# Kernel optimization log

Hardware: AMD Instinct MI355X
Metric: run time of the kernel (lower is better)

The kernel has to match this reference:

```python
import jax, jax.numpy as jnp
import numpy as np

T, B, I, H, O = 4096, 256, 2, 32, 1


def setup_inputs() -> dict:
    key = jax.random.key(0)
    ks = jax.random.split(key, 8)
    s = 1.0 / np.sqrt(H)  # torch GRU/Linear init scale
    u = lambda k, shape: jax.random.uniform(k, shape, jnp.float32, -s, s)
    return {
        "x": jax.random.normal(ks[0], (T, B, I), jnp.float32),
        "w_ih": u(ks[1], (3 * H, I)),   # rows ordered [r, z, n] as in torch
        "w_hh": u(ks[2], (3 * H, H)),
        "b_ih": u(ks[3], (3 * H,)),
        "b_hh": u(ks[4], (3 * H,)),
        "w_fc": u(ks[5], (O, H)),
        "b_fc": u(ks[6], (O,)),
    }


def _gru_all_hidden(x, w_ih, w_hh, b_ih, b_hh):
    # Precompute input projections for all steps in one big GEMM: (T,B,3H)
    xg = jnp.einsum('tbi,gi->tbg', x, w_ih) + b_ih

    def step(h, xg_t):
        hg = h @ w_hh.T + b_hh                      # (B,3H)
        xr, xz, xn = jnp.split(xg_t, 3, axis=-1)
        hr, hz, hn = jnp.split(hg, 3, axis=-1)
        r = jax.nn.sigmoid(xr + hr)
        z = jax.nn.sigmoid(xz + hz)
        n = jnp.tanh(xn + r * hn)
        h_new = (1.0 - z) * n + z * h
        return h_new, h_new

    h0 = jnp.zeros((x.shape[1], w_hh.shape[1]), x.dtype)
    _, hs = jax.lax.scan(step, h0, xg)
    return hs                                       # (T,B,H)


def reference(x, w_ih, w_hh, b_ih, b_hh, w_fc, b_fc):
    hs = _gru_all_hidden(x, w_ih, w_hh, b_ih, b_hh)  # (T,B,H)
    # Faithful to the source: output[:, -1, :] with batch_first=False picks
    # the last batch element's hidden state at every timestep -> (T,H)
    out = hs[:, -1, :]
    return out @ w_fc.T + b_fc                       # (T,O)
```

## Files before the change

### kernel.cpp

```cpp
#include <hip/hip_runtime.h>


#define TT 4096

__device__ __forceinline__ float rl(float v, int l) {
    return __int_as_float(__builtin_amdgcn_readlane(__float_as_int(v), l));
}
__device__ __forceinline__ float fexp2(float x) { return __builtin_amdgcn_exp2f(x); }
__device__ __forceinline__ float frcp(float x)  { return __builtin_amdgcn_rcpf(x); }

#define NLOG2E  (-1.44269504088896340736f)
#define TLOG2E  ( 2.88539008177792681472f)

__global__ __launch_bounds__(64, 1)
__attribute__((amdgpu_waves_per_eu(1, 1)))
void gru_seq(const float* __restrict__ x,
             const float* __restrict__ w_ih,
             const float* __restrict__ w_hh,
             const float* __restrict__ b_ih,
             const float* __restrict__ b_hh,
             float* __restrict__ hbuf)
{
    const int lane = threadIdx.x;
    const int low  = lane & 31;
    const bool hi  = lane >= 32;
    const int row0 = lane;
    const int row1 = 64 + low;

    float w0a[32], w1a[32];
#pragma unroll
    for (int j = 0; j < 32; ++j) w0a[j] = w_hh[row0 * 32 + j] * NLOG2E;
#pragma unroll
    for (int j = 0; j < 32; ++j) w1a[j] = w_hh[row1 * 32 + j] * TLOG2E;
#pragma unroll
    for (int j = 0; j < 32; ++j) asm("" : "+v"(w0a[j]));
#pragma unroll
    for (int j = 0; j < 32; ++j) asm("" : "+v"(w1a[j]));

    const float wi00 = w_ih[row0 * 2 + 0] * NLOG2E;
    const float wi01 = w_ih[row0 * 2 + 1] * NLOG2E;
    const float wi10 = w_ih[row1 * 2 + 0] * TLOG2E;
    const float wi11 = w_ih[row1 * 2 + 1] * TLOG2E;
    const float bias0 = (b_ih[row0] + b_hh[row0]) * NLOG2E;
    const float bi1   = b_ih[row1] * TLOG2E;
    const float bh1   = b_hh[row1] * TLOG2E;

    float h_el = 0.0f;
    float hs[32];
#pragma unroll
    for (int j = 0; j < 32; ++j) hs[j] = 0.0f;

    const float2* xp = (const float2*)x;
    float2 xv = xp[(size_t)lane * 256 + 255];
    float hacc[4];

    for (int tb = 0; tb < 64; ++tb) {
        float2 xv_next = xv;
        if (tb < 63) xv_next = xp[((size_t)(tb + 1) * 64 + lane) * 256 + 255];
        float4* hout = (float4*)(hbuf + (size_t)low * TT + tb * 64);

#pragma unroll 4
        for (int i = 0; i < 64; ++i) {
            const float x0 = rl(xv.x, i);
            const float x1 = rl(xv.y, i);
            float a = fmaf(x1, wi01, fmaf(x0, wi00, bias0));
            float b = 0.f, c = 0.f, d = 0.f;
            const float xn = fmaf(x1, wi11, fmaf(x0, wi10, bi1));
            float n0 = bh1, n1 = 0.f, n2 = 0.f, n3 = 0.f;

#pragma unroll
            for (int j = 0; j < 32; j += 4) {
                a  = fmaf(hs[j + 0], w0a[j + 0], a);
                b  = fmaf(hs[j + 1], w0a[j + 1], b);
                c  = fmaf(hs[j + 2], w0a[j + 2], c);
                d  = fmaf(hs[j + 3], w0a[j + 3], d);
                n0 = fmaf(hs[j + 0], w1a[j + 0], n0);
                n1 = fmaf(hs[j + 1], w1a[j + 1], n1);
                n2 = fmaf(hs[j + 2], w1a[j + 2], n2);
                n3 = fmaf(hs[j + 3], w1a[j + 3], n3);
            }
            const float pre_s = (a + b) + (c + d);
            const float hn_s  = (n0 + n1) + (n2 + n3);

            const float sg    = frcp(1.0f + fexp2(pre_s));
            const float other = __shfl_xor(sg, 32);
            const float rr = hi ? other : sg;
            const float zz = hi ? sg : other;

            const float nv = fmaf(-2.0f, frcp(1.0f + fexp2(fmaf(rr, hn_s, xn))), 1.0f);
            h_el = fmaf(zz, h_el - nv, nv);

            hacc[i & 3] = h_el;
            if ((i & 3) == 3) hout[i >> 2] = *(const float4*)hacc;

#pragma unroll
            for (int j = 0; j < 32; ++j) hs[j] = rl(h_el, j);
        }
        xv = xv_next;
    }
}

__global__ void fc_out(const float* __restrict__ hbuf,
                       const float* __restrict__ w_fc,
                       const float* __restrict__ b_fc,
                       float* __restrict__ out)
{
    const int t = blockIdx.x * blockDim.x + threadIdx.x;
    if (t >= TT) return;
    float acc = 0.f;
#pragma unroll
    for (int j = 0; j < 32; ++j) acc = fmaf(hbuf[j * TT + t], w_fc[j], acc);
    out[t] = acc + b_fc[0];
}

extern "C" void kernel_launch(void* const* d_in, const int* in_sizes, int n_in,
                              void* d_out, int out_size, void* d_ws, size_t ws_size,
                              hipStream_t stream) {
    const float* x    = (const float*)d_in[0];
    const float* w_ih = (const float*)d_in[1];
    const float* w_hh = (const float*)d_in[2];
    const float* b_ih = (const float*)d_in[3];
    const float* b_hh = (const float*)d_in[4];
    const float* w_fc = (const float*)d_in[5];
    const float* b_fc = (const float*)d_in[6];
    float* out  = (float*)d_out;
    float* hbuf = (float*)d_ws;

    gru_seq<<<1, 64, 0, stream>>>(x, w_ih, w_hh, b_ih, b_hh, hbuf);
    fc_out<<<TT / 256, 256, 0, stream>>>(hbuf, w_fc, b_fc, out);
}
```

Before: 880.2 us.

## Use packed fp16 dot2 for recurrent matvec with DPP pair packing

Stores the recurrent weights as packed half pairs and computes the per-step 32-wide dot products with v_dot2 fp32-accumulate instructions, which halves the FMA count. Hidden-state broadcast now packs neighbouring lanes into half2 via a DPP swap and cvt_pkrtz, so 16 readlanes are needed instead of 32. It also drops the waves_per_eu attribute and the register-pinning asm. In exchange, the weights and hidden state are rounded to fp16 at every step, which adds error that can build up over 4096 recurrent steps.

```diff
diff --git a/kernel.cpp b/kernel.cpp
--- a/kernel.cpp
+++ b/kernel.cpp
@@ -3,17 +3,22 @@
 
 #define TT 4096
 
+typedef _Float16 h2 __attribute__((ext_vector_type(2)));
+
 __device__ __forceinline__ float rl(float v, int l) {
     return __int_as_float(__builtin_amdgcn_readlane(__float_as_int(v), l));
 }
+__device__ __forceinline__ int rli(int v, int l) {
+    return __builtin_amdgcn_readlane(v, l);
+}
 __device__ __forceinline__ float fexp2(float x) { return __builtin_amdgcn_exp2f(x); }
 __device__ __forceinline__ float frcp(float x)  { return __builtin_amdgcn_rcpf(x); }
+__device__ __forceinline__ h2 asph(int v) { return __builtin_bit_cast(h2, v); }
 
 #define NLOG2E  (-1.44269504088896340736f)
 #define TLOG2E  ( 2.88539008177792681472f)
 
 __global__ __launch_bounds__(64, 1)
-__attribute__((amdgpu_waves_per_eu(1, 1)))
 void gru_seq(const float* __restrict__ x,
              const float* __restrict__ w_ih,
              const float* __restrict__ w_hh,
@@ -27,15 +32,19 @@
     const int row0 = lane;
     const int row1 = 64 + low;
 
-    float w0a[32], w1a[32];
+    h2 w0p[16], w1p[16];
 #pragma unroll
-    for (int j = 0; j < 32; ++j) w0a[j] = w_hh[row0 * 32 + j] * NLOG2E;
+    for (int m = 0; m < 16; ++m) {
+        float a = w_hh[row0 * 32 + 2 * m] * NLOG2E;
+        float b = w_hh[row0 * 32 + 2 * m + 1] * NLOG2E;
+        w0p[m] = h2{(_Float16)a, (_Float16)b};
+    }
 #pragma unroll
-    for (int j = 0; j < 32; ++j) w1a[j] = w_hh[row1 * 32 + j] * TLOG2E;
-#pragma unroll
-    for (int j = 0; j < 32; ++j) asm("" : "+v"(w0a[j]));
-#pragma unroll
-    for (int j = 0; j < 32; ++j) asm("" : "+v"(w1a[j]));
+    for (int m = 0; m < 16; ++m) {
+        float a = w_hh[row1 * 32 + 2 * m] * TLOG2E;
+        float b = w_hh[row1 * 32 + 2 * m + 1] * TLOG2E;
+        w1p[m] = h2{(_Float16)a, (_Float16)b};
+    }
 
     const float wi00 = w_ih[row0 * 2 + 0] * NLOG2E;
     const float wi01 = w_ih[row0 * 2 + 1] * NLOG2E;
@@ -46,13 +55,14 @@
     const float bh1   = b_hh[row1] * TLOG2E;
 
     float h_el = 0.0f;
-    float hs[32];
+    int hsp[16];
 #pragma unroll
-    for (int j = 0; j < 32; ++j) hs[j] = 0.0f;
+    for (int m = 0; m < 16; ++m) hsp[m] = 0;
 
     const float2* xp = (const float2*)x;
     float2 xv = xp[(size_t)lane * 256 + 255];
     float hacc[4];
+    const int odd = lane & 1;
 
     for (int tb = 0; tb < 64; ++tb) {
         float2 xv_next = xv;
@@ -63,24 +73,22 @@
         for (int i = 0; i < 64; ++i) {
             const float x0 = rl(xv.x, i);
             const float x1 = rl(xv.y, i);
-            float a = fmaf(x1, wi01, fmaf(x0, wi00, bias0));
-            float b = 0.f, c = 0.f, d = 0.f;
-            const float xn = fmaf(x1, wi11, fmaf(x0, wi10, bi1));
-            float n0 = bh1, n1 = 0.f, n2 = 0.f, n3 = 0.f;
+            const float base0 = fmaf(x1, wi01, fmaf(x0, wi00, bias0));
+            const float xn    = fmaf(x1, wi11, fmaf(x0, wi10, bi1));
 
+            float a0 = base0, a1 = 0.f;
+            float n0 = bh1,   n1 = 0.f;
 #pragma unroll
-            for (int j = 0; j < 32; j += 4) {
-                a  = fmaf(hs[j + 0], w0a[j + 0], a);
-                b  = fmaf(hs[j + 1], w0a[j + 1], b);
-                c  = fmaf(hs[j + 2], w0a[j + 2], c);
-                d  = fmaf(hs[j + 3], w0a[j + 3], d);
-                n0 = fmaf(hs[j + 0], w1a[j + 0], n0);
-                n1 = fmaf(hs[j + 1], w1a[j + 1], n1);
-                n2 = fmaf(hs[j + 2], w1a[j + 2], n2);
-                n3 = fmaf(hs[j + 3], w1a[j + 3], n3);
+            for (int m = 0; m < 16; m += 2) {
+                const h2 hA = asph(hsp[m]);
+                const h2 hB = asph(hsp[m + 1]);
+                a0 = __builtin_amdgcn_fdot2(w0p[m],     hA, a0, false);
+                a1 = __builtin_amdgcn_fdot2(w0p[m + 1], hB, a1, false);
+                n0 = __builtin_amdgcn_fdot2(w1p[m],     hA, n0, false);
+                n1 = __builtin_amdgcn_fdot2(w1p[m + 1], hB, n1, false);
             }
-            const float pre_s = (a + b) + (c + d);
-            const float hn_s  = (n0 + n1) + (n2 + n3);
+            const float pre_s = a0 + a1;
+            const float hn_s  = n0 + n1;
 
             const float sg    = frcp(1.0f + fexp2(pre_s));
             const float other = __shfl_xor(sg, 32);
@@ -93,8 +101,13 @@
             hacc[i & 3] = h_el;
             if ((i & 3) == 3) hout[i >> 2] = *(const float4*)hacc;
 
+            const float nb = __int_as_float(__builtin_amdgcn_update_dpp(
+                0, __float_as_int(h_el), 0xB1, 0xF, 0xF, true));
+            const float pa = odd ? nb : h_el;
+            const float pb = odd ? h_el : nb;
+            const int pk = __builtin_bit_cast(int, __builtin_amdgcn_cvt_pkrtz(pa, pb));
 #pragma unroll
-            for (int j = 0; j < 32; ++j) hs[j] = rl(h_el, j);
+            for (int m = 0; m < 16; ++m) hsp[m] = rli(pk, 2 * m);
         }
         xv = xv_next;
     }
```

Measured after the change: 776.8 us. -11.7%, faster.
